# Kernel tuning notes

Hardware: AMD Instinct MI355X
Metric: run time of the kernel (lower is better)

The kernel has to match this reference:

```python
import jax, jax.numpy as jnp
import numpy as np

H = 50  # hidden_size

def setup_inputs() -> dict:
    key = jax.random.key(0)
    ks = jax.random.split(key, 7)
    B, T = 2048, 1024
    s = 1.0 / np.sqrt(H)  # PyTorch default init scale
    return {
        "x": jax.random.normal(ks[0], (B, T, 1), dtype=jnp.float32),
        "W_ih": jax.random.uniform(ks[1], (4 * H, 1), jnp.float32, -s, s),
        "W_hh": jax.random.uniform(ks[2], (4 * H, H), jnp.float32, -s, s),
        "b_ih": jax.random.uniform(ks[3], (4 * H,), jnp.float32, -s, s),
        "b_hh": jax.random.uniform(ks[4], (4 * H,), jnp.float32, -s, s),
        "W_lin": jax.random.uniform(ks[5], (1, H), jnp.float32, -s, s),
        "b_lin": jax.random.uniform(ks[6], (1,), jnp.float32, -s, s),
    }

def reference(x, W_ih, W_hh, b_ih, b_hh, W_lin, b_lin):
    B, T, _ = x.shape
    # Precompute input contribution to gates for all timesteps: [T, B, 4H]
    gx = jnp.einsum('bti,gi->tbg', x, W_ih) + (b_ih + b_hh)

    def step(carry, gx_t):
        h, c = carry
        gates = gx_t + h @ W_hh.T               # [B, 4H]
        i, f, g, o = jnp.split(gates, 4, axis=-1)  # PyTorch gate order i,f,g,o
        i = jax.nn.sigmoid(i)
        f = jax.nn.sigmoid(f)
        g = jnp.tanh(g)
        o = jax.nn.sigmoid(o)
        c = f * c + i * g
        h = o * jnp.tanh(c)
        return (h, c), None

    h0 = jnp.zeros((B, H), x.dtype)
    c0 = jnp.zeros((B, H), x.dtype)
    (h_last, _), _ = jax.lax.scan(step, (h0, c0), gx)
    # Linear head on last timestep's hidden state -> [B, 1]
    return h_last @ W_lin.T + b_lin
```

## Files before the change

kernel.cpp:

```cpp
#include <hip/hip_runtime.h>


#define H     50
#define TT    1024
#define BATCH 2048
#define BW    8
#define NTHR  448
#define KP    80

typedef float    f32x4 __attribute__((ext_vector_type(4)));
typedef _Float16 f16x8 __attribute__((ext_vector_type(8)));

__global__ __launch_bounds__(NTHR, 1) void lstm_kernel(
    const float* __restrict__ x,
    const float* __restrict__ W_ih,
    const float* __restrict__ W_hh,
    const float* __restrict__ b_ih,
    const float* __restrict__ b_hh,
    const float* __restrict__ W_lin,
    const float* __restrict__ b_lin,
    float* __restrict__ out)
{
    __shared__ _Float16 hb[2][BW][KP];
    __shared__ float    XT[TT + 2][BW];
    __shared__ float    redH[H][BW];

    const int tid  = threadIdx.x;
    const int wave = tid >> 6;
    const int lane = tid & 63;
    const int L15  = lane & 15;
    const int kq   = lane >> 4;
    const int bl   = L15 & 7;
    const int b0   = blockIdx.x * BW;
    const int t0   = 2 * wave;

    const float LOG2E  = 1.4426950408889634f;
    const float LOG2E2 = 2.8853900817779268f;

    f16x8 A[2][2];
    #pragma unroll
    for (int tt = 0; tt < 2; ++tt) {
        const int m  = (t0 + tt) * 16 + L15;
        const int jm = m >> 2, gm = m & 3;
        const bool v = (jm < H);
        const float s = (gm == 2) ? LOG2E2 : -LOG2E;
        #pragma unroll
        for (int kf = 0; kf < 2; ++kf) {
            f16x8 vv;
            #pragma unroll
            for (int e = 0; e < 8; ++e) {
                const int k = kf * 32 + kq * 8 + e;
                _Float16 val = (_Float16)0.f;
                if (v && k < H) val = (_Float16)(s * W_hh[(gm * H + jm) * H + k]);
                vv[e] = val;
            }
            A[tt][kf] = vv;
        }
    }

    const int  j  = 8 * wave + ((L15 >> 3) << 2) + kq;
    const bool jv = (j < H);
    const float wlin = jv ? W_lin[j] : 0.f;
    float zw[4], zb[4];
    #pragma unroll
    for (int r = 0; r < 4; ++r) {
        const float s = (r == 2) ? LOG2E2 : -LOG2E;
        zw[r] = jv ? s * W_ih[r * H + j] : 0.f;
        zb[r] = jv ? s * (b_ih[r * H + j] + b_hh[r * H + j]) : 0.f;
    }

    for (int i = tid; i < 2 * BW * KP; i += NTHR)
        ((_Float16*)hb)[i] = (_Float16)0.f;
    for (int i = tid; i < TT * BW; i += NTHR) {
        const int bb = i >> 10, t = i & 1023;
        XT[t][bb] = x[(size_t)(b0 + bb) * TT + t];
    }
    if (tid < 2 * BW) ((float*)&XT[TT][0])[tid] = 0.f;

    float c2 = 0.f;
    float hlast = 0.f;
    __syncthreads();

    float xt_cur = XT[0][bl];
    const bool lo = (L15 < 8);

    #pragma unroll 1
    for (int tbase = 0; tbase < TT; tbase += 2) {
        #pragma unroll
        for (int half = 0; half < 2; ++half) {
            const int t = tbase + half;
            const _Float16* hp = &hb[half][bl][0];
            _Float16*       np = &hb[half ^ 1][bl][0];

            const f16x8 B0 = *(const f16x8*)(hp + kq * 8);
            const f16x8 B1 = *(const f16x8*)(hp + 32 + kq * 8);

            f32x4 zc;
            #pragma unroll
            for (int r = 0; r < 4; ++r)
                zc[r] = __builtin_fmaf(zw[r], xt_cur, zb[r]);
            const f32x4 zz = {0.f, 0.f, 0.f, 0.f};

            f32x4 a0 = __builtin_amdgcn_mfma_f32_16x16x32_f16(A[0][0], B0, zc, 0, 0, 0);
            f32x4 a1 = __builtin_amdgcn_mfma_f32_16x16x32_f16(A[1][0], B0, zc, 0, 0, 0);
            f32x4 p0 = __builtin_amdgcn_mfma_f32_16x16x32_f16(A[0][1], B1, zz, 0, 0, 0);
            f32x4 p1 = __builtin_amdgcn_mfma_f32_16x16x32_f16(A[1][1], B1, zz, 0, 0, 0);

            xt_cur = XT[t + 1][bl];

            const float gi = lo ? (a0[0] + p0[0]) : (a1[0] + p1[0]);
            const float gf = lo ? (a0[1] + p0[1]) : (a1[1] + p1[1]);
            const float gg = lo ? (a0[2] + p0[2]) : (a1[2] + p1[2]);
            const float go = lo ? (a0[3] + p0[3]) : (a1[3] + p1[3]);

            const float Ei = __builtin_amdgcn_exp2f(gi);
            const float Ef = __builtin_amdgcn_exp2f(gf);
            const float Eg = __builtin_amdgcn_exp2f(gg);
            const float Eo = __builtin_amdgcn_exp2f(go);
            const float P  = (1.0f + Ei) * (1.0f + Eg);
            const float Q  = 1.0f + Ef;
            const float Q2 = __builtin_fmaf(LOG2E2, Ef, LOG2E2);
            const float num = __builtin_fmaf(c2, P, (Eg - 1.0f) * Q2);
            c2 = num * __builtin_amdgcn_rcpf(P * Q);
            const float ca = fminf(c2, 80.0f);
            const float Ec = __builtin_amdgcn_exp2f(ca);
            const float h  = (Ec - 1.0f) *
                __builtin_amdgcn_rcpf((1.0f + Eo) * (1.0f + Ec));
            hlast = h;

            np[j] = (_Float16)h;
            __syncthreads();
        }
    }

    if (jv) redH[j][bl] = wlin * hlast;
    __syncthreads();
    if (tid < BW) {
        float s = b_lin[0];
        #pragma unroll 10
        for (int jj = 0; jj < H; ++jj) s += redH[jj][tid];
        out[b0 + tid] = s;
    }
}

extern "C" void kernel_launch(void* const* d_in, const int* in_sizes, int n_in,
                              void* d_out, int out_size, void* d_ws, size_t ws_size,
                              hipStream_t stream) {
    const float* x     = (const float*)d_in[0];
    const float* W_ih  = (const float*)d_in[1];
    const float* W_hh  = (const float*)d_in[2];
    const float* b_ih  = (const float*)d_in[3];
    const float* b_hh  = (const float*)d_in[4];
    const float* W_lin = (const float*)d_in[5];
    const float* b_lin = (const float*)d_in[6];
    float* out = (float*)d_out;

    dim3 grid(BATCH / BW);
    dim3 block(NTHR);
    lstm_kernel<<<grid, block, 0, stream>>>(x, W_ih, W_hh, b_ih, b_hh,
                                            W_lin, b_lin, out);
}
```

Measured before the change: 350.5 us.

## Halve batch per block, give each wave four gate tiles, chain MFMA accumulators

Each block now handles 4 batch rows with 256 threads (4 waves), and each wave computes four 16-row gate tiles instead of two, so a 200-row gate matrix fits in fewer waves. The K-split MFMAs now accumulate into the same register instead of summing two separate partial results. Launch bounds allow two blocks per CU, and there are twice as many blocks, so more independent recurrences can be in flight to hide the per-step barrier and MFMA latency. The cost is longer serial MFMA dependency chains per wave and half the batch columns of each MFMA left unused.

New measurement: 338.7 us. -3.3%, faster.

```diff
diff --git a/kernel.cpp b/kernel.cpp
--- a/kernel.cpp
+++ b/kernel.cpp
@@ -4,14 +4,15 @@
 #define H     50
 #define TT    1024
 #define BATCH 2048
-#define BW    8
-#define NTHR  448
+#define BW    4
+#define NTHR  256
+#define NTILE 4
 #define KP    80
 
 typedef float    f32x4 __attribute__((ext_vector_type(4)));
 typedef _Float16 f16x8 __attribute__((ext_vector_type(8)));
 
-__global__ __launch_bounds__(NTHR, 1) void lstm_kernel(
+__global__ __launch_bounds__(NTHR, 2) void lstm_kernel(
     const float* __restrict__ x,
     const float* __restrict__ W_ih,
     const float* __restrict__ W_hh,
@@ -30,17 +31,16 @@
     const int lane = tid & 63;
     const int L15  = lane & 15;
     const int kq   = lane >> 4;
-    const int bl   = L15 & 7;
+    const int bl   = L15 & 3;
     const int b0   = blockIdx.x * BW;
-    const int t0   = 2 * wave;
 
     const float LOG2E  = 1.4426950408889634f;
     const float LOG2E2 = 2.8853900817779268f;
 
-    f16x8 A[2][2];
+    f16x8 A[NTILE][2];
     #pragma unroll
-    for (int tt = 0; tt < 2; ++tt) {
-        const int m  = (t0 + tt) * 16 + L15;
+    for (int tt = 0; tt < NTILE; ++tt) {
+        const int m  = (NTILE * wave + tt) * 16 + L15;
         const int jm = m >> 2, gm = m & 3;
         const bool v = (jm < H);
         const float s = (gm == 2) ? LOG2E2 : -LOG2E;
@@ -58,7 +58,7 @@
         }
     }
 
-    const int  j  = 8 * wave + ((L15 >> 3) << 2) + kq;
+    const int  j  = 16 * wave + 4 * (L15 >> 2) + kq;
     const bool jv = (j < H);
     const float wlin = jv ? W_lin[j] : 0.f;
     float zw[4], zb[4];
@@ -82,7 +82,8 @@
     __syncthreads();
 
     float xt_cur = XT[0][bl];
-    const bool lo = (L15 < 8);
+    const bool s0 = (L15 & 4) != 0;
+    const bool s1 = (L15 & 8) != 0;
 
     #pragma unroll 1
     for (int tbase = 0; tbase < TT; tbase += 2) {
@@ -99,24 +100,30 @@
             #pragma unroll
             for (int r = 0; r < 4; ++r)
                 zc[r] = __builtin_fmaf(zw[r], xt_cur, zb[r]);
-            const f32x4 zz = {0.f, 0.f, 0.f, 0.f};
 
             f32x4 a0 = __builtin_amdgcn_mfma_f32_16x16x32_f16(A[0][0], B0, zc, 0, 0, 0);
             f32x4 a1 = __builtin_amdgcn_mfma_f32_16x16x32_f16(A[1][0], B0, zc, 0, 0, 0);
-            f32x4 p0 = __builtin_amdgcn_mfma_f32_16x16x32_f16(A[0][1], B1, zz, 0, 0, 0);
-            f32x4 p1 = __builtin_amdgcn_mfma_f32_16x16x32_f16(A[1][1], B1, zz, 0, 0, 0);
+            f32x4 a2 = __builtin_amdgcn_mfma_f32_16x16x32_f16(A[2][0], B0, zc, 0, 0, 0);
+            f32x4 a3 = __builtin_amdgcn_mfma_f32_16x16x32_f16(A[3][0], B0, zc, 0, 0, 0);
+            a0 = __builtin_amdgcn_mfma_f32_16x16x32_f16(A[0][1], B1, a0, 0, 0, 0);
+            a1 = __builtin_amdgcn_mfma_f32_16x16x32_f16(A[1][1], B1, a1, 0, 0, 0);
+            a2 = __builtin_amdgcn_mfma_f32_16x16x32_f16(A[2][1], B1, a2, 0, 0, 0);
+            a3 = __builtin_amdgcn_mfma_f32_16x16x32_f16(A[3][1], B1, a3, 0, 0, 0);
 
             xt_cur = XT[t + 1][bl];
 
-            const float gi = lo ? (a0[0] + p0[0]) : (a1[0] + p1[0]);
-            const float gf = lo ? (a0[1] + p0[1]) : (a1[1] + p1[1]);
-            const float gg = lo ? (a0[2] + p0[2]) : (a1[2] + p1[2]);
-            const float go = lo ? (a0[3] + p0[3]) : (a1[3] + p1[3]);
+            float g[4];
+            #pragma unroll
+            for (int r = 0; r < 4; ++r) {
+                const float m01 = s0 ? a1[r] : a0[r];
+                const float m23 = s0 ? a3[r] : a2[r];
+                g[r] = s1 ? m23 : m01;
+            }
 
-            const float Ei = __builtin_amdgcn_exp2f(gi);
-            const float Ef = __builtin_amdgcn_exp2f(gf);
-            const float Eg = __builtin_amdgcn_exp2f(gg);
-            const float Eo = __builtin_amdgcn_exp2f(go);
+            const float Ei = __builtin_amdgcn_exp2f(g[0]);
+            const float Ef = __builtin_amdgcn_exp2f(g[1]);
+            const float Eg = __builtin_amdgcn_exp2f(g[2]);
+            const float Eo = __builtin_amdgcn_exp2f(g[3]);
             const float P  = (1.0f + Ei) * (1.0f + Eg);
             const float Q  = 1.0f + Ef;
             const float Q2 = __builtin_fmaf(LOG2E2, Ef, LOG2E2);
```

## Run each LSTM batch slice in a single wave with bpermute hidden-state exchange

Applied to the files above, without the earlier changes.

Each block now holds one 64-lane wavefront covering 2 batch rows instead of 7 waves covering 8. All 13 W_hh tiles stay in registers, and the hidden state passes between lanes through ds_bpermute instead of shared memory. This removes the per-timestep __syncthreads and the LDS round trip from the serial recurrence. In exchange each wave issues 26 MFMAs per step, uses far more registers, and the grid grows to 1024 single-wave blocks, which may underuse the MFMA units because each batch column is padded to 16.

Measured after the change: 625.4 us. +78.4%, slower.

```diff
diff --git a/kernel.cpp b/kernel.cpp
--- a/kernel.cpp
+++ b/kernel.cpp
@@ -4,14 +4,14 @@
 #define H     50
 #define TT    1024
 #define BATCH 2048
-#define BW    8
-#define NTHR  448
-#define KP    80
-
-typedef float    f32x4 __attribute__((ext_vector_type(4)));
-typedef _Float16 f16x8 __attribute__((ext_vector_type(8)));
-
-__global__ __launch_bounds__(NTHR, 1) void lstm_kernel(
+#define BW    2
+#define NT    13
+
+typedef float        f32x4 __attribute__((ext_vector_type(4)));
+typedef _Float16     f16x8 __attribute__((ext_vector_type(8)));
+typedef unsigned int u32x4 __attribute__((ext_vector_type(4)));
+
+__global__ __launch_bounds__(64, 1) void lstm_kernel(
     const float* __restrict__ x,
     const float* __restrict__ W_ih,
     const float* __restrict__ W_hh,
@@ -21,26 +21,22 @@
     const float* __restrict__ b_lin,
     float* __restrict__ out)
 {
-    __shared__ _Float16 hb[2][BW][KP];
-    __shared__ float    XT[TT + 2][BW];
-    __shared__ float    redH[H][BW];
-
-    const int tid  = threadIdx.x;
-    const int wave = tid >> 6;
-    const int lane = tid & 63;
+    __shared__ float XT[TT + 1][BW];
+
+    const int lane = threadIdx.x & 63;
+    const int kq   = lane >> 4;
     const int L15  = lane & 15;
-    const int kq   = lane >> 4;
-    const int bl   = L15 & 7;
+    const int ts   = L15 >> 1;
+    const int bl   = L15 & 1;
     const int b0   = blockIdx.x * BW;
-    const int t0   = 2 * wave;
 
     const float LOG2E  = 1.4426950408889634f;
     const float LOG2E2 = 2.8853900817779268f;
 
-    f16x8 A[2][2];
-    #pragma unroll
-    for (int tt = 0; tt < 2; ++tt) {
-        const int m  = (t0 + tt) * 16 + L15;
+    f16x8 A[NT][2];
+    #pragma unroll
+    for (int tt = 0; tt < NT; ++tt) {
+        const int m  = tt * 16 + L15;
         const int jm = m >> 2, gm = m & 3;
         const bool v = (jm < H);
         const float s = (gm == 2) ? LOG2E2 : -LOG2E;
@@ -48,99 +44,142 @@
         for (int kf = 0; kf < 2; ++kf) {
             f16x8 vv;
             #pragma unroll
-            for (int e = 0; e < 8; ++e) {
-                const int k = kf * 32 + kq * 8 + e;
+            for (int p = 0; p < 8; ++p) {
+                const int kap = 8 * kq + 4 * kf + (p >> 1) + 32 * (p & 1);
                 _Float16 val = (_Float16)0.f;
-                if (v && k < H) val = (_Float16)(s * W_hh[(gm * H + jm) * H + k]);
-                vv[e] = val;
+                if (v && kap < H) val = (_Float16)(s * W_hh[(gm * H + jm) * H + kap]);
+                vv[p] = val;
             }
             A[tt][kf] = vv;
         }
     }
 
-    const int  j  = 8 * wave + ((L15 >> 3) << 2) + kq;
-    const bool jv = (j < H);
-    const float wlin = jv ? W_lin[j] : 0.f;
-    float zw[4], zb[4];
+    const int  j0  = 4 * ts + kq;
+    const int  j1  = 32 + 4 * ts + kq;
+    const bool jv1 = (j1 < H);
+    float zw0[4], zb0[4], zw1[4], zb1[4];
     #pragma unroll
     for (int r = 0; r < 4; ++r) {
         const float s = (r == 2) ? LOG2E2 : -LOG2E;
-        zw[r] = jv ? s * W_ih[r * H + j] : 0.f;
-        zb[r] = jv ? s * (b_ih[r * H + j] + b_hh[r * H + j]) : 0.f;
-    }
-
-    for (int i = tid; i < 2 * BW * KP; i += NTHR)
-        ((_Float16*)hb)[i] = (_Float16)0.f;
-    for (int i = tid; i < TT * BW; i += NTHR) {
-        const int bb = i >> 10, t = i & 1023;
+        zw0[r] = s * W_ih[r * H + j0];
+        zb0[r] = s * (b_ih[r * H + j0] + b_hh[r * H + j0]);
+        zw1[r] = jv1 ? s * W_ih[r * H + j1] : 0.f;
+        zb1[r] = jv1 ? s * (b_ih[r * H + j1] + b_hh[r * H + j1]) : 0.f;
+    }
+    const float wl0 = W_lin[j0];
+    const float wl1 = jv1 ? W_lin[j1] : 0.f;
+
+    int gaddr[8];
+    #pragma unroll
+    for (int e = 0; e < 8; ++e) {
+        const int src = 16 * (e & 3) + 2 * (2 * kq + (e >> 2)) + bl;
+        gaddr[e] = src << 2;
+    }
+
+    for (int i = lane; i < TT * BW; i += 64) {
+        const int bb = i >> 10, t = i & (TT - 1);
         XT[t][bb] = x[(size_t)(b0 + bb) * TT + t];
     }
-    if (tid < 2 * BW) ((float*)&XT[TT][0])[tid] = 0.f;
-
-    float c2 = 0.f;
-    float hlast = 0.f;
+    if (lane < BW) XT[TT][lane] = 0.f;
     __syncthreads();
 
+    float c2a = 0.f, c2b = 0.f;
+    float h0f = 0.f, h1f = 0.f;
+    int   P0  = 0;
     float xt_cur = XT[0][bl];
-    const bool lo = (L15 < 8);
+
+    const bool tb0 = (ts & 1) != 0;
+    const bool tb1 = (ts & 2) != 0;
+    const bool tb2 = (ts & 4) != 0;
 
     #pragma unroll 1
-    for (int tbase = 0; tbase < TT; tbase += 2) {
-        #pragma unroll
-        for (int half = 0; half < 2; ++half) {
-            const int t = tbase + half;
-            const _Float16* hp = &hb[half][bl][0];
-            _Float16*       np = &hb[half ^ 1][bl][0];
-
-            const f16x8 B0 = *(const f16x8*)(hp + kq * 8);
-            const f16x8 B1 = *(const f16x8*)(hp + 32 + kq * 8);
-
-            f32x4 zc;
-            #pragma unroll
-            for (int r = 0; r < 4; ++r)
-                zc[r] = __builtin_fmaf(zw[r], xt_cur, zb[r]);
-            const f32x4 zz = {0.f, 0.f, 0.f, 0.f};
-
-            f32x4 a0 = __builtin_amdgcn_mfma_f32_16x16x32_f16(A[0][0], B0, zc, 0, 0, 0);
-            f32x4 a1 = __builtin_amdgcn_mfma_f32_16x16x32_f16(A[1][0], B0, zc, 0, 0, 0);
-            f32x4 p0 = __builtin_amdgcn_mfma_f32_16x16x32_f16(A[0][1], B1, zz, 0, 0, 0);
-            f32x4 p1 = __builtin_amdgcn_mfma_f32_16x16x32_f16(A[1][1], B1, zz, 0, 0, 0);
-
-            xt_cur = XT[t + 1][bl];
-
-            const float gi = lo ? (a0[0] + p0[0]) : (a1[0] + p1[0]);
-            const float gf = lo ? (a0[1] + p0[1]) : (a1[1] + p1[1]);
-            const float gg = lo ? (a0[2] + p0[2]) : (a1[2] + p1[2]);
-            const float go = lo ? (a0[3] + p0[3]) : (a1[3] + p1[3]);
-
-            const float Ei = __builtin_amdgcn_exp2f(gi);
-            const float Ef = __builtin_amdgcn_exp2f(gf);
-            const float Eg = __builtin_amdgcn_exp2f(gg);
-            const float Eo = __builtin_amdgcn_exp2f(go);
+    for (int t = 0; t < TT; ++t) {
+        int g[8];
+        #pragma unroll
+        for (int e = 0; e < 8; ++e)
+            g[e] = __builtin_amdgcn_ds_bpermute(gaddr[e], P0);
+        const float xt_nxt = XT[t + 1][bl];
+
+        float gz0[4], gz1[4];
+        #pragma unroll
+        for (int r = 0; r < 4; ++r) {
+            gz0[r] = __builtin_fmaf(zw0[r], xt_cur, zb0[r]);
+            gz1[r] = __builtin_fmaf(zw1[r], xt_cur, zb1[r]);
+        }
+
+        u32x4 b0w, b1w;
+        b0w[0] = g[0]; b0w[1] = g[1]; b0w[2] = g[2]; b0w[3] = g[3];
+        b1w[0] = g[4]; b1w[1] = g[5]; b1w[2] = g[6]; b1w[3] = g[7];
+        const f16x8 Bh0 = __builtin_bit_cast(f16x8, b0w);
+        const f16x8 Bh1 = __builtin_bit_cast(f16x8, b1w);
+
+        const f32x4 zz = {0.f, 0.f, 0.f, 0.f};
+        f32x4 acc[NT];
+        #pragma unroll
+        for (int tt = 0; tt < NT; ++tt)
+            acc[tt] = __builtin_amdgcn_mfma_f32_16x16x32_f16(A[tt][0], Bh0, zz, 0, 0, 0);
+        #pragma unroll
+        for (int tt = 0; tt < NT; ++tt)
+            acc[tt] = __builtin_amdgcn_mfma_f32_16x16x32_f16(A[tt][1], Bh1, acc[tt], 0, 0, 0);
+
+        float ga[4], gb[4];
+        #pragma unroll
+        for (int r = 0; r < 4; ++r) {
+            const float m01 = tb0 ? acc[1][r]  : acc[0][r];
+            const float m23 = tb0 ? acc[3][r]  : acc[2][r];
+            const float m45 = tb0 ? acc[5][r]  : acc[4][r];
+            const float m67 = tb0 ? acc[7][r]  : acc[6][r];
+            const float m03 = tb1 ? m23 : m01;
+            const float m47 = tb1 ? m67 : m45;
+            ga[r] = (tb2 ? m47 : m03) + gz0[r];
+
+            const float n89 = tb0 ? acc[9][r]  : acc[8][r];
+            const float nAB = tb0 ? acc[11][r] : acc[10][r];
+            const float n8B = tb1 ? nAB : n89;
+            gb[r] = (tb2 ? acc[12][r] : n8B) + gz1[r];
+        }
+
+        {
+            const float Ei = __builtin_amdgcn_exp2f(ga[0]);
+            const float Ef = __builtin_amdgcn_exp2f(ga[1]);
+            const float Eg = __builtin_amdgcn_exp2f(ga[2]);
+            const float Eo = __builtin_amdgcn_exp2f(ga[3]);
             const float P  = (1.0f + Ei) * (1.0f + Eg);
             const float Q  = 1.0f + Ef;
             const float Q2 = __builtin_fmaf(LOG2E2, Ef, LOG2E2);
-            const float num = __builtin_fmaf(c2, P, (Eg - 1.0f) * Q2);
-            c2 = num * __builtin_amdgcn_rcpf(P * Q);
-            const float ca = fminf(c2, 80.0f);
+            const float num = __builtin_fmaf(c2a, P, (Eg - 1.0f) * Q2);
+            c2a = num * __builtin_amdgcn_rcpf(P * Q);
+            const float ca = fminf(c2a, 80.0f);
             const float Ec = __builtin_amdgcn_exp2f(ca);
-            const float h  = (Ec - 1.0f) *
-                __builtin_amdgcn_rcpf((1.0f + Eo) * (1.0f + Ec));
-            hlast = h;
-
-            np[j] = (_Float16)h;
-            __syncthreads();
-        }
-    }
-
-    if (jv) redH[j][bl] = wlin * hlast;
-    __syncthreads();
-    if (tid < BW) {
-        float s = b_lin[0];
-        #pragma unroll 10
-        for (int jj = 0; jj < H; ++jj) s += redH[jj][tid];
-        out[b0 + tid] = s;
-    }
+            h0f = (Ec - 1.0f) * __builtin_amdgcn_rcpf((1.0f + Eo) * (1.0f + Ec));
+        }
+        {
+            const float Ei = __builtin_amdgcn_exp2f(gb[0]);
+            const float Ef = __builtin_amdgcn_exp2f(gb[1]);
+            const float Eg = __builtin_amdgcn_exp2f(gb[2]);
+            const float Eo = __builtin_amdgcn_exp2f(gb[3]);
+            const float P  = (1.0f + Ei) * (1.0f + Eg);
+            const float Q  = 1.0f + Ef;
+            const float Q2 = __builtin_fmaf(LOG2E2, Ef, LOG2E2);
+            const float num = __builtin_fmaf(c2b, P, (Eg - 1.0f) * Q2);
+            c2b = num * __builtin_amdgcn_rcpf(P * Q);
+            const float ca = fminf(c2b, 80.0f);
+            const float Ec = __builtin_amdgcn_exp2f(ca);
+            h1f = (Ec - 1.0f) * __builtin_amdgcn_rcpf((1.0f + Eo) * (1.0f + Ec));
+        }
+
+        const _Float16 hh0 = (_Float16)h0f;
+        const _Float16 hh1 = jv1 ? (_Float16)h1f : (_Float16)0.f;
+        const unsigned int u0 = (unsigned int)__builtin_bit_cast(unsigned short, hh0);
+        const unsigned int u1 = (unsigned int)__builtin_bit_cast(unsigned short, hh1);
+        P0 = (int)(u0 | (u1 << 16));
+        xt_cur = xt_nxt;
+    }
+
+    float p = __builtin_fmaf(wl0, h0f, wl1 * h1f);
+    #pragma unroll
+    for (int m = 2; m <= 32; m <<= 1) p += __shfl_xor(p, m, 64);
+    if (lane < BW) out[b0 + lane] = p + b_lin[0];
 }
 
 extern "C" void kernel_launch(void* const* d_in, const int* in_sizes, int n_in,
@@ -156,7 +195,7 @@
     float* out = (float*)d_out;
 
     dim3 grid(BATCH / BW);
-    dim3 block(NTHR);
+    dim3 block(64);
     lstm_kernel<<<grid, block, 0, stream>>>(x, W_ih, W_hh, b_ih, b_hh,
                                             W_lin, b_lin, out);
 }
```
